# Kernel tuning notes

Measured on AMD Instinct MI355X. Metric: run time of the kernel, lower is better.

Reference implementation:

```python
import jax, jax.numpy as jnp
import numpy as np

B, N, E, FN = 4, 10000, 320000, 16
E_H, E_H2, E_OUT, N_H, N_OUT = 64, 32, 64, 12, 1
IN_DIM = 2 * FN + 1  # node_src + node_target + edge_weight


def _linear_params(key, fan_in, fan_out):
    k1, k2 = jax.random.split(key)
    bound = 1.0 / np.sqrt(fan_in)
    W = jax.random.uniform(k1, (fan_in, fan_out), jnp.float32, -bound, bound)
    b = jax.random.uniform(k2, (fan_out,), jnp.float32, -bound, bound)
    return W, b


def setup_inputs() -> dict:
    key = jax.random.key(0)
    ks = jax.random.split(key, 10)
    node_features = jax.random.normal(ks[0], (B, N, FN), jnp.float32)
    edge_weight = jax.random.uniform(ks[1], (B, E), jnp.float32)
    label_prev = jax.random.uniform(ks[2], (B, N, 1), jnp.float32)
    edge_src = jax.random.randint(ks[3], (E,), 0, N, jnp.int64)
    edge_target = jax.random.randint(ks[4], (E,), 0, N, jnp.int64)
    W1, b1 = _linear_params(ks[5], IN_DIM, E_H)
    W2, b2 = _linear_params(ks[6], E_H, E_H2)
    W3, b3 = _linear_params(ks[7], E_H2, E_OUT)
    W4, b4 = _linear_params(ks[8], E_OUT + 1, N_H)
    W5, b5 = _linear_params(ks[9], N_H, N_OUT)
    return {
        "node_features": node_features, "edge_weight": edge_weight,
        "label_prev": label_prev, "edge_src": edge_src, "edge_target": edge_target,
        "W1": W1, "b1": b1, "W2": W2, "b2": b2, "W3": W3, "b3": b3,
        "W4": W4, "b4": b4, "W5": W5, "b5": b5,
    }


def reference(node_features, edge_weight, label_prev, edge_src, edge_target,
              W1, b1, W2, b2, W3, b3, W4, b4, W5, b5):
    # Gather endpoint features per edge: [B, E, FN]
    node_src = node_features[:, edge_src]
    node_tgt = node_features[:, edge_target]
    e_in = jnp.concatenate([node_src, node_tgt, edge_weight[..., None]], axis=-1)  # [B,E,33]
    # Edge MLP (dropout in eval mode = identity)
    h = jax.nn.relu(e_in @ W1 + b1)
    h = jax.nn.relu(h @ W2 + b2)
    h = jax.nn.sigmoid(h @ W3 + b3)  # [B, E, 64]
    # scatter_add to targets, scatter_add of -h to sources
    n_nodes = node_features.shape[1]
    agg = (jnp.zeros((h.shape[0], n_nodes, h.shape[-1]), h.dtype)
           .at[:, edge_target].add(h)
           .at[:, edge_src].add(-h))  # [B, N, 64]
    lp = label_prev.reshape(agg.shape[0], n_nodes, 1)
    n_in = jnp.concatenate([agg, lp], axis=-1)  # [B, N, 65]
    # Node MLP
    n = jax.nn.relu(n_in @ W4 + b4)
    out = jax.nn.sigmoid(n @ W5 + b5)  # [B, N, 1]
    return out
```

## Files before the change

kernel.cpp:

```cpp
#include <hip/hip_runtime.h>
#include <cstdint>
#include <cstddef>

#define B_    4
#define N_    10000
#define E_    320000
#define FN_   16
#define INDIM 33
#define EH    64
#define EH2   32
#define EOUT  64
#define NHID  12

__device__ __forceinline__ float f4get(const float4& v, int k) {
    switch (k) { case 0: return v.x; case 1: return v.y; case 2: return v.z; default: return v.w; }
}
__device__ __forceinline__ void fma4(float4& a, float s, const float4 w) {
    a.x = fmaf(s, w.x, a.x); a.y = fmaf(s, w.y, a.y);
    a.z = fmaf(s, w.z, a.z); a.w = fmaf(s, w.w, a.w);
}
__device__ __forceinline__ void relu4(float4& a) {
    a.x = fmaxf(a.x, 0.f); a.y = fmaxf(a.y, 0.f);
    a.z = fmaxf(a.z, 0.f); a.w = fmaxf(a.w, 0.f);
}

__global__ __launch_bounds__(256, 2) void edge_kernel(
    const float* __restrict__ nf,
    const float* __restrict__ ew,
    const int*   __restrict__ esrc,
    const int*   __restrict__ etgt,
    const float* __restrict__ W1, const float* __restrict__ b1,
    const float* __restrict__ W2, const float* __restrict__ b2,
    const float* __restrict__ W3, const float* __restrict__ b3,
    float* __restrict__ agg)
{
    __shared__ float sW1[INDIM * EH];
    __shared__ float sb1[EH];
    __shared__ float sW2[EH * EH2];
    __shared__ float sb2[EH2];
    __shared__ float sh2[4][64][36];
    __shared__ int   sidx[4][64][2];

    const int tid = threadIdx.x;
    const int b   = blockIdx.y;

    for (int i = tid; i < INDIM * EH; i += 256) sW1[i] = W1[i];
    for (int i = tid; i < EH * EH2;   i += 256) sW2[i] = W2[i];
    if (tid < EH)  sb1[tid] = b1[tid];
    if (tid < EH2) sb2[tid] = b2[tid];

    const int e   = blockIdx.x * 256 + tid;
    const int src = esrc[e];
    const int tgt = etgt[e];
    const float w = ew[(size_t)b * E_ + e];

    float4 inv[8];
    {
        const float4* ps = (const float4*)(nf + ((size_t)b * N_ + src) * FN_);
        const float4* pt = (const float4*)(nf + ((size_t)b * N_ + tgt) * FN_);
        inv[0] = ps[0]; inv[1] = ps[1]; inv[2] = ps[2]; inv[3] = ps[3];
        inv[4] = pt[0]; inv[5] = pt[1]; inv[6] = pt[2]; inv[7] = pt[3];
    }

    __syncthreads();

    float4 h1[16];
    {
        const float4* bv = (const float4*)sb1;
        #pragma unroll
        for (int j = 0; j < 16; j++) h1[j] = bv[j];
    }
    #pragma unroll
    for (int i = 0; i < 32; i++) {
        float v = f4get(inv[i >> 2], i & 3);
        const float4* wr = (const float4*)(sW1 + i * EH);
        #pragma unroll
        for (int j = 0; j < 16; j++) fma4(h1[j], v, wr[j]);
    }
    {
        const float4* wr = (const float4*)(sW1 + 32 * EH);
        #pragma unroll
        for (int j = 0; j < 16; j++) fma4(h1[j], w, wr[j]);
    }
    #pragma unroll
    for (int j = 0; j < 16; j++) relu4(h1[j]);

    float4 h2[8];
    {
        const float4* bv = (const float4*)sb2;
        #pragma unroll
        for (int j = 0; j < 8; j++) h2[j] = bv[j];
    }
    #pragma unroll
    for (int i = 0; i < 64; i++) {
        float v = f4get(h1[i >> 2], i & 3);
        const float4* wr = (const float4*)(sW2 + i * EH2);
        #pragma unroll
        for (int j = 0; j < 8; j++) fma4(h2[j], v, wr[j]);
    }
    #pragma unroll
    for (int j = 0; j < 8; j++) relu4(h2[j]);

    const int wv = tid >> 6, ln = tid & 63;
    {
        float4* dst = (float4*)&sh2[wv][ln][0];
        #pragma unroll
        for (int j = 0; j < 8; j++) dst[j] = h2[j];
        sidx[wv][ln][0] = src;
        sidx[wv][ln][1] = tgt;
    }

    float w3c[32];
    #pragma unroll
    for (int i = 0; i < 32; i++) w3c[i] = W3[i * EOUT + ln];
    const float bias3 = b3[ln];

    __syncthreads();

    float* aggB = agg + (size_t)b * N_ * EOUT;
    for (int ee = 0; ee < 64; ee++) {
        const float4* hp = (const float4*)&sh2[wv][ee][0];
        float acc = bias3;
        #pragma unroll
        for (int c = 0; c < 8; c++) {
            float4 hh = hp[c];
            acc = fmaf(hh.x, w3c[4 * c + 0], acc);
            acc = fmaf(hh.y, w3c[4 * c + 1], acc);
            acc = fmaf(hh.z, w3c[4 * c + 2], acc);
            acc = fmaf(hh.w, w3c[4 * c + 3], acc);
        }
        float s = 1.0f / (1.0f + __expf(-acc));
        int t2 = sidx[wv][ee][1];
        int s2 = sidx[wv][ee][0];
        atomicAdd(aggB + (size_t)t2 * EOUT + ln,  s);
        atomicAdd(aggB + (size_t)s2 * EOUT + ln, -s);
    }
}

__global__ __launch_bounds__(256) void node_kernel(
    const float* __restrict__ agg,
    const float* __restrict__ lp,
    const float* __restrict__ W4, const float* __restrict__ b4,
    const float* __restrict__ W5, const float* __restrict__ b5,
    float* __restrict__ out)
{
    __shared__ float sW4[65 * NHID];
    __shared__ float sb4[NHID];
    __shared__ float sW5[NHID];
    __shared__ float sb5;

    const int tid = threadIdx.x;
    for (int i = tid; i < 65 * NHID; i += 256) sW4[i] = W4[i];
    if (tid < NHID) { sb4[tid] = b4[tid]; sW5[tid] = W5[tid]; }
    if (tid == 0) sb5 = b5[0];
    __syncthreads();

    const int idx = blockIdx.x * 256 + tid;
    if (idx >= B_ * N_) return;

    float nh[NHID];
    #pragma unroll
    for (int j = 0; j < NHID; j++) nh[j] = sb4[j];

    const float4* ar = (const float4*)(agg + (size_t)idx * EOUT);
    #pragma unroll
    for (int c = 0; c < 16; c++) {
        float4 a4 = ar[c];
        #pragma unroll
        for (int k = 0; k < 4; k++) {
            float v = f4get(a4, k);
            const float* wr = sW4 + (c * 4 + k) * NHID;
            #pragma unroll
            for (int j = 0; j < NHID; j++) nh[j] = fmaf(v, wr[j], nh[j]);
        }
    }
    {
        float v = lp[idx];
        const float* wr = sW4 + 64 * NHID;
        #pragma unroll
        for (int j = 0; j < NHID; j++) nh[j] = fmaf(v, wr[j], nh[j]);
    }

    float acc = sb5;
    #pragma unroll
    for (int j = 0; j < NHID; j++) acc = fmaf(fmaxf(nh[j], 0.f), sW5[j], acc);
    out[idx] = 1.0f / (1.0f + __expf(-acc));
}

extern "C" void kernel_launch(void* const* d_in, const int* in_sizes, int n_in,
                              void* d_out, int out_size, void* d_ws, size_t ws_size,
                              hipStream_t stream)
{
    const float* nf   = (const float*)d_in[0];
    const float* ew   = (const float*)d_in[1];
    const float* lp   = (const float*)d_in[2];
    const int*   esrc = (const int*)d_in[3];
    const int*   etgt = (const int*)d_in[4];
    const float* W1 = (const float*)d_in[5],  *b1 = (const float*)d_in[6];
    const float* W2 = (const float*)d_in[7],  *b2 = (const float*)d_in[8];
    const float* W3 = (const float*)d_in[9],  *b3 = (const float*)d_in[10];
    const float* W4 = (const float*)d_in[11], *b4 = (const float*)d_in[12];
    const float* W5 = (const float*)d_in[13], *b5 = (const float*)d_in[14];

    float* out = (float*)d_out;
    float* agg = (float*)d_ws;

    const size_t aggBytes = (size_t)B_ * N_ * EOUT * sizeof(float);
    hipMemsetAsync(agg, 0, aggBytes, stream);

    dim3 eg(E_ / 256, B_);
    edge_kernel<<<eg, 256, 0, stream>>>(nf, ew, esrc, etgt,
                                        W1, b1, W2, b2, W3, b3, agg);

    node_kernel<<<(B_ * N_ + 255) / 256, 256, 0, stream>>>(agg, lp, W4, b4, W5, b5, out);
}
```

Baseline: 630.9 us.

## Replace global atomic scatter with bucketed CSR-style aggregation and fp16 edge outputs

```diff
diff --git a/kernel.cpp b/kernel.cpp
--- a/kernel.cpp
+++ b/kernel.cpp
@@ -2,15 +2,18 @@
 #include <cstdint>
 #include <cstddef>
 
-#define B_    4
-#define N_    10000
-#define E_    320000
-#define FN_   16
-#define INDIM 33
-#define EH    64
-#define EH2   32
-#define EOUT  64
-#define NHID  12
+#define B_     4
+#define N_     10000
+#define E_     320000
+#define FN_    16
+#define INDIM  33
+#define EH     64
+#define EH2    32
+#define EOUT   64
+#define NHID   12
+#define CH2    32
+#define NCHUNK2 313
+
 
 __device__ __forceinline__ float f4get(const float4& v, int k) {
     switch (k) { case 0: return v.x; case 1: return v.y; case 2: return v.z; default: return v.w; }
@@ -24,7 +27,52 @@
     a.z = fmaxf(a.z, 0.f); a.w = fmaxf(a.w, 0.f);
 }
 
-__global__ __launch_bounds__(256, 2) void edge_kernel(
+
+__global__ __launch_bounds__(256) void hist_kernel(
+    const int* __restrict__ esrc, const int* __restrict__ etgt,
+    int* __restrict__ counts)
+{
+    __shared__ int hc[NCHUNK2];
+    const int tid = threadIdx.x;
+    for (int i = tid; i < NCHUNK2; i += 256) hc[i] = 0;
+    __syncthreads();
+    const int e = blockIdx.x * 256 + tid;
+    atomicAdd(&hc[esrc[e] >> 5], 1);
+    atomicAdd(&hc[etgt[e] >> 5], 1);
+    __syncthreads();
+    for (int i = tid; i < NCHUNK2; i += 256)
+        if (hc[i]) atomicAdd(&counts[i], hc[i]);
+}
+
+__global__ void scan_kernel(const int* __restrict__ counts,
+                            int* __restrict__ offsets,
+                            int* __restrict__ cursors)
+{
+    if (threadIdx.x == 0) {
+        int acc = 0;
+        for (int i = 0; i < NCHUNK2; i++) {
+            offsets[i] = acc;
+            cursors[i] = acc;
+            acc += counts[i];
+        }
+        offsets[NCHUNK2] = acc;
+    }
+}
+
+__global__ __launch_bounds__(256) void fill_kernel(
+    const int* __restrict__ esrc, const int* __restrict__ etgt,
+    int* __restrict__ cursors, unsigned* __restrict__ entries)
+{
+    const int e = blockIdx.x * 256 + threadIdx.x;
+    const int s = esrc[e], t = etgt[e];
+    int p = atomicAdd(&cursors[s >> 5], 1);
+    entries[p] = (unsigned)e | (1u << 19) | ((unsigned)(s & 31) << 20);
+    p = atomicAdd(&cursors[t >> 5], 1);
+    entries[p] = (unsigned)e | ((unsigned)(t & 31) << 20);
+}
+
+
+__global__ __launch_bounds__(256, 3) void edge_h_kernel(
     const float* __restrict__ nf,
     const float* __restrict__ ew,
     const int*   __restrict__ esrc,
@@ -32,6 +80,198 @@
     const float* __restrict__ W1, const float* __restrict__ b1,
     const float* __restrict__ W2, const float* __restrict__ b2,
     const float* __restrict__ W3, const float* __restrict__ b3,
+    _Float16* __restrict__ h16,
+    int bbase)
+{
+    __shared__ float sW1[INDIM * EH];
+    __shared__ float sb1[EH];
+    __shared__ float sW2[EH * EH2];
+    __shared__ float sb2[EH2];
+    __shared__ float sh2[4][64][36];
+
+    const int tid = threadIdx.x;
+    const int hb  = blockIdx.y;
+    const int b   = bbase + hb;
+
+    for (int i = tid; i < INDIM * EH; i += 256) sW1[i] = W1[i];
+    for (int i = tid; i < EH * EH2;   i += 256) sW2[i] = W2[i];
+    if (tid < EH)  sb1[tid] = b1[tid];
+    if (tid < EH2) sb2[tid] = b2[tid];
+
+    const int e   = blockIdx.x * 256 + tid;
+    const int src = esrc[e];
+    const int tgt = etgt[e];
+    const float w = ew[(size_t)b * E_ + e];
+
+    float4 inv[8];
+    {
+        const float4* ps = (const float4*)(nf + ((size_t)b * N_ + src) * FN_);
+        const float4* pt = (const float4*)(nf + ((size_t)b * N_ + tgt) * FN_);
+        inv[0] = ps[0]; inv[1] = ps[1]; inv[2] = ps[2]; inv[3] = ps[3];
+        inv[4] = pt[0]; inv[5] = pt[1]; inv[6] = pt[2]; inv[7] = pt[3];
+    }
+
+    __syncthreads();
+
+    float4 h1[16];
+    {
+        const float4* bv = (const float4*)sb1;
+        #pragma unroll
+        for (int j = 0; j < 16; j++) h1[j] = bv[j];
+    }
+    #pragma unroll
+    for (int i = 0; i < 32; i++) {
+        float v = f4get(inv[i >> 2], i & 3);
+        const float4* wr = (const float4*)(sW1 + i * EH);
+        #pragma unroll
+        for (int j = 0; j < 16; j++) fma4(h1[j], v, wr[j]);
+    }
+    {
+        const float4* wr = (const float4*)(sW1 + 32 * EH);
+        #pragma unroll
+        for (int j = 0; j < 16; j++) fma4(h1[j], w, wr[j]);
+    }
+    #pragma unroll
+    for (int j = 0; j < 16; j++) relu4(h1[j]);
+
+    float4 h2[8];
+    {
+        const float4* bv = (const float4*)sb2;
+        #pragma unroll
+        for (int j = 0; j < 8; j++) h2[j] = bv[j];
+    }
+    #pragma unroll
+    for (int i = 0; i < 64; i++) {
+        float v = f4get(h1[i >> 2], i & 3);
+        const float4* wr = (const float4*)(sW2 + i * EH2);
+        #pragma unroll
+        for (int j = 0; j < 8; j++) fma4(h2[j], v, wr[j]);
+    }
+    #pragma unroll
+    for (int j = 0; j < 8; j++) relu4(h2[j]);
+
+    const int wv = tid >> 6, ln = tid & 63;
+    {
+        float4* dst = (float4*)&sh2[wv][ln][0];
+        #pragma unroll
+        for (int j = 0; j < 8; j++) dst[j] = h2[j];
+    }
+
+    float w3c[32];
+    #pragma unroll
+    for (int i = 0; i < 32; i++) w3c[i] = W3[i * EOUT + ln];
+    const float bias3 = b3[ln];
+
+    __syncthreads();
+
+    const int e0 = blockIdx.x * 256 + wv * 64;
+    _Float16* hout = h16 + ((size_t)hb * E_ + e0) * EOUT + ln;
+    for (int ee = 0; ee < 64; ee++) {
+        const float4* hp = (const float4*)&sh2[wv][ee][0];
+        float acc = bias3;
+        #pragma unroll
+        for (int cc = 0; cc < 8; cc++) {
+            float4 hh = hp[cc];
+            acc = fmaf(hh.x, w3c[4 * cc + 0], acc);
+            acc = fmaf(hh.y, w3c[4 * cc + 1], acc);
+            acc = fmaf(hh.z, w3c[4 * cc + 2], acc);
+            acc = fmaf(hh.w, w3c[4 * cc + 3], acc);
+        }
+        float s = 1.0f / (1.0f + __expf(-acc));
+        hout[(size_t)ee * EOUT] = (_Float16)s;
+    }
+}
+
+
+__global__ __launch_bounds__(256) void aggregate_kernel(
+    const _Float16* __restrict__ h16,
+    const float* __restrict__ lp,
+    const unsigned* __restrict__ entries,
+    const int* __restrict__ offsets,
+    const float* __restrict__ W4, const float* __restrict__ b4,
+    const float* __restrict__ W5, const float* __restrict__ b5,
+    float* __restrict__ out,
+    int bbase)
+{
+    __shared__ float sagg[CH2][68];
+    __shared__ float sW4[(EOUT + 1) * NHID];
+    __shared__ float sb4[NHID];
+    __shared__ float sW5[NHID];
+    __shared__ float sb5v;
+
+    const int tid = threadIdx.x;
+    const int c   = blockIdx.x;
+    const int hb  = blockIdx.y;
+    const int b   = bbase + hb;
+    const int node0  = c * CH2;
+    const int nvalid = min(CH2, N_ - node0);
+
+    for (int i = tid; i < (EOUT + 1) * NHID; i += 256) sW4[i] = W4[i];
+    if (tid < NHID) { sb4[tid] = b4[tid]; sW5[tid] = W5[tid]; }
+    if (tid == 0) sb5v = b5[0];
+    {
+        float* sa = &sagg[0][0];
+        for (int i = tid; i < CH2 * 68; i += 256) sa[i] = 0.f;
+    }
+    __syncthreads();
+
+    const int beg = offsets[c], end = offsets[c + 1];
+    const int wv = tid >> 6, ln = tid & 63;
+    const _Float16* hbase = h16 + (size_t)hb * E_ * EOUT + ln;
+
+    for (int it = beg + wv * 4; it < end; it += 16) {
+        const int n0 = min(4, end - it);
+        unsigned ent[4];
+        float    hv[4];
+        #pragma unroll
+        for (int k = 0; k < 4; k++)
+            if (k < n0) ent[k] = entries[it + k];
+        #pragma unroll
+        for (int k = 0; k < 4; k++)
+            if (k < n0) hv[k] = (float)hbase[(size_t)(ent[k] & 0x7FFFFu) * EOUT];
+        #pragma unroll
+        for (int k = 0; k < 4; k++)
+            if (k < n0) {
+                float s = ((ent[k] >> 19) & 1u) ? -hv[k] : hv[k];
+                atomicAdd(&sagg[(ent[k] >> 20) & 31u][ln], s);
+            }
+    }
+
+    __syncthreads();
+
+    if (tid < nvalid) {
+        float nh[NHID];
+        #pragma unroll
+        for (int j = 0; j < NHID; j++) nh[j] = sb4[j];
+
+        const float* ar = &sagg[tid][0];
+        #pragma unroll
+        for (int k = 0; k < EOUT; k++) {
+            float v = ar[k];
+            const float* wr = sW4 + k * NHID;
+            #pragma unroll
+            for (int j = 0; j < NHID; j++) nh[j] = fmaf(v, wr[j], nh[j]);
+        }
+        {
+            float v = lp[(size_t)b * N_ + node0 + tid];
+            const float* wr = sW4 + EOUT * NHID;
+            #pragma unroll
+            for (int j = 0; j < NHID; j++) nh[j] = fmaf(v, wr[j], nh[j]);
+        }
+        float acc = sb5v;
+        #pragma unroll
+        for (int j = 0; j < NHID; j++) acc = fmaf(fmaxf(nh[j], 0.f), sW5[j], acc);
+        out[(size_t)b * N_ + node0 + tid] = 1.0f / (1.0f + __expf(-acc));
+    }
+}
+
+
+__global__ __launch_bounds__(256, 2) void edge_kernel_legacy(
+    const float* __restrict__ nf, const float* __restrict__ ew,
+    const int* __restrict__ esrc, const int* __restrict__ etgt,
+    const float* __restrict__ W1, const float* __restrict__ b1,
+    const float* __restrict__ W2, const float* __restrict__ b2,
+    const float* __restrict__ W3, const float* __restrict__ b3,
     float* __restrict__ agg)
 {
     __shared__ float sW1[INDIM * EH];
@@ -61,7 +301,6 @@
         inv[0] = ps[0]; inv[1] = ps[1]; inv[2] = ps[2]; inv[3] = ps[3];
         inv[4] = pt[0]; inv[5] = pt[1]; inv[6] = pt[2]; inv[7] = pt[3];
     }
-
     __syncthreads();
 
     float4 h1[16];
@@ -122,12 +361,12 @@
         const float4* hp = (const float4*)&sh2[wv][ee][0];
         float acc = bias3;
         #pragma unroll
-        for (int c = 0; c < 8; c++) {
-            float4 hh = hp[c];
-            acc = fmaf(hh.x, w3c[4 * c + 0], acc);
-            acc = fmaf(hh.y, w3c[4 * c + 1], acc);
-            acc = fmaf(hh.z, w3c[4 * c + 2], acc);
-            acc = fmaf(hh.w, w3c[4 * c + 3], acc);
+        for (int cc = 0; cc < 8; cc++) {
+            float4 hh = hp[cc];
+            acc = fmaf(hh.x, w3c[4 * cc + 0], acc);
+            acc = fmaf(hh.y, w3c[4 * cc + 1], acc);
+            acc = fmaf(hh.z, w3c[4 * cc + 2], acc);
+            acc = fmaf(hh.w, w3c[4 * cc + 3], acc);
         }
         float s = 1.0f / (1.0f + __expf(-acc));
         int t2 = sidx[wv][ee][1];
@@ -137,9 +376,8 @@
     }
 }
 
-__global__ __launch_bounds__(256) void node_kernel(
-    const float* __restrict__ agg,
-    const float* __restrict__ lp,
+__global__ __launch_bounds__(256) void node_kernel_legacy(
+    const float* __restrict__ agg, const float* __restrict__ lp,
     const float* __restrict__ W4, const float* __restrict__ b4,
     const float* __restrict__ W5, const float* __restrict__ b5,
     float* __restrict__ out)
@@ -180,12 +418,12 @@
         #pragma unroll
         for (int j = 0; j < NHID; j++) nh[j] = fmaf(v, wr[j], nh[j]);
     }
-
     float acc = sb5;
     #pragma unroll
     for (int j = 0; j < NHID; j++) acc = fmaf(fmaxf(nh[j], 0.f), sW5[j], acc);
     out[idx] = 1.0f / (1.0f + __expf(-acc));
 }
+
 
 extern "C" void kernel_launch(void* const* d_in, const int* in_sizes, int n_in,
                               void* d_out, int out_size, void* d_ws, size_t ws_size,
@@ -203,14 +441,49 @@
     const float* W5 = (const float*)d_in[13], *b5 = (const float*)d_in[14];
 
     float* out = (float*)d_out;
-    float* agg = (float*)d_ws;
-
-    const size_t aggBytes = (size_t)B_ * N_ * EOUT * sizeof(float);
-    hipMemsetAsync(agg, 0, aggBytes, stream);
-
-    dim3 eg(E_ / 256, B_);
-    edge_kernel<<<eg, 256, 0, stream>>>(nf, ew, esrc, etgt,
-                                        W1, b1, W2, b2, W3, b3, agg);
-
-    node_kernel<<<(B_ * N_ + 255) / 256, 256, 0, stream>>>(agg, lp, W4, b4, W5, b5, out);
-}
+    char*  ws  = (char*)d_ws;
+
+    const size_t H_OFF      = 4u << 20;
+    const size_t H_BATCH    = (size_t)E_ * EOUT * sizeof(_Float16);
+    const size_t NEED_FULL  = H_OFF + (size_t)B_ * H_BATCH;
+    const size_t NEED_BATCH = H_OFF + H_BATCH;
+
+    if (ws_size >= NEED_BATCH) {
+        int*      counts  = (int*)(ws + 0);
+        int*      offsets = (int*)(ws + 2048);
+        int*      cursors = (int*)(ws + 4096);
+        unsigned* entries = (unsigned*)(ws + 8192);
+        _Float16* h16     = (_Float16*)(ws + H_OFF);
+
+        hipMemsetAsync(counts, 0, 2048, stream);
+        hist_kernel<<<E_ / 256, 256, 0, stream>>>(esrc, etgt, counts);
+        scan_kernel<<<1, 64, 0, stream>>>(counts, offsets, cursors);
+        fill_kernel<<<E_ / 256, 256, 0, stream>>>(esrc, etgt, cursors, entries);
+
+        if (ws_size >= NEED_FULL) {
+            dim3 ga(E_ / 256, B_);
+            edge_h_kernel<<<ga, 256, 0, stream>>>(nf, ew, esrc, etgt,
+                                                  W1, b1, W2, b2, W3, b3, h16, 0);
+            dim3 gb(NCHUNK2, B_);
+            aggregate_kernel<<<gb, 256, 0, stream>>>(h16, lp, entries, offsets,
+                                                     W4, b4, W5, b5, out, 0);
+        } else {
+            for (int b = 0; b < B_; b++) {
+                dim3 ga(E_ / 256, 1);
+                edge_h_kernel<<<ga, 256, 0, stream>>>(nf, ew, esrc, etgt,
+                                                      W1, b1, W2, b2, W3, b3, h16, b);
+                dim3 gb(NCHUNK2, 1);
+                aggregate_kernel<<<gb, 256, 0, stream>>>(h16, lp, entries, offsets,
+                                                         W4, b4, W5, b5, out, b);
+            }
+        }
+    } else {
+        float* agg = (float*)d_ws;
+        hipMemsetAsync(agg, 0, (size_t)B_ * N_ * EOUT * sizeof(float), stream);
+        dim3 eg(E_ / 256, B_);
+        edge_kernel_legacy<<<eg, 256, 0, stream>>>(nf, ew, esrc, etgt,
+                                                   W1, b1, W2, b2, W3, b3, agg);
+        node_kernel_legacy<<<(B_ * N_ + 255) / 256, 256, 0, stream>>>(agg, lp,
+                                                   W4, b4, W5, b5, out);
+    }
+}
```

Result: slower. 1.547 ms (+145.2%).
